# Kernel tuning notes

Measured on AMD Instinct MI355X. Metric: run time of the kernel, lower is better.

The kernel has to match this reference:

```python
import jax, jax.numpy as jnp
import numpy as np

N_EMBD = 1024
HEAD_SIZE = 64


def setup_inputs() -> dict:
    key = jax.random.key(0)
    kx, kq, kk, kv = jax.random.split(key, 4)
    B, T = 8, 2048
    x = jax.random.normal(kx, (B, T, N_EMBD), dtype=jnp.float32)
    s = 1.0 / np.sqrt(N_EMBD)
    Wq = jax.random.normal(kq, (N_EMBD, HEAD_SIZE), dtype=jnp.float32) * s
    Wk = jax.random.normal(kk, (N_EMBD, HEAD_SIZE), dtype=jnp.float32) * s
    Wv = jax.random.normal(kv, (N_EMBD, HEAD_SIZE), dtype=jnp.float32) * s
    return {"x": x, "Wq": Wq, "Wk": Wk, "Wv": Wv}


def reference(x, Wq, Wk, Wv):
    # x: [B, T, C]; W*: [C, H]
    q = jnp.einsum('btc,ch->bth', x, Wq)
    k = jnp.einsum('btc,ch->bth', x, Wk)
    v = jnp.einsum('btc,ch->bth', x, Wv)
    H = q.shape[-1]
    score = jnp.einsum('bth,bsh->bts', q, k) / jnp.sqrt(jnp.asarray(H, q.dtype))
    T = score.shape[-1]
    causal = jnp.tril(jnp.ones((T, T), dtype=bool))  # [T, T]
    score = jnp.where(causal, score, -jnp.inf)
    attn = jax.nn.softmax(score, axis=-1)
    return jnp.einsum('bts,bsh->bth', attn, v)
```

## Files before the change

kernel.cpp:

```cpp
#include <hip/hip_runtime.h>

typedef __bf16 bf16;
typedef __attribute__((ext_vector_type(8))) __bf16 bf16x8;
typedef __attribute__((ext_vector_type(4))) __bf16 bf16x4;
typedef __attribute__((ext_vector_type(4))) float floatx4;

#define MFMA16(a, b, c) __builtin_amdgcn_mfma_f32_16x16x32_bf16((a), (b), (c), 0, 0, 0)

__global__ void prep_w(const float* __restrict__ Wq, const float* __restrict__ Wk,
                       const float* __restrict__ Wv, bf16* __restrict__ wTf) {
    int tid = blockIdx.x * 256 + threadIdx.x;
    int j = tid & 7;
    int l = (tid >> 3) & 15;
    int q = (tid >> 7) & 3;
    int kc = (tid >> 9) & 31;
    int mt = tid >> 14;
    int mat = mt >> 2;
    int h = ((mt & 3) << 4) + l;
    int c = kc * 32 + q * 8 + j;
    const float* W = (mat == 0) ? Wq : (mat == 1) ? Wk : Wv;
    wTf[tid] = (bf16)W[c * 64 + h];
}

#define XSTR 1032

__global__ __launch_bounds__(256, 4) void proj_qkv(const float* __restrict__ x,
                                                   const bf16* __restrict__ wTf,
                                                   bf16* __restrict__ q,
                                                   bf16* __restrict__ k,
                                                   bf16* __restrict__ vT) {
    __shared__ bf16 xs[16 * XSTR];

    const int tid = threadIdx.x;
    const int lane = tid & 63;
    const int w = tid >> 6;
    const int l15 = lane & 15;
    const int quad = lane >> 4;
    const int T0 = blockIdx.x * 16;

    {
        const int r = tid >> 4;
        const int cm = tid & 15;
        const float* g = x + (size_t)(T0 + r) * 1024 + cm * 8;
        floatx4 f[16];
        #pragma unroll
        for (int c = 0; c < 8; c++) {
            f[2 * c]     = *(const floatx4*)(g + c * 128);
            f[2 * c + 1] = *(const floatx4*)(g + c * 128 + 4);
        }
        bf16* ld = xs + r * XSTR + cm * 8;
        #pragma unroll
        for (int c = 0; c < 8; c++) {
            bf16x8 pk;
            pk[0] = (bf16)f[2*c][0]; pk[1] = (bf16)f[2*c][1];
            pk[2] = (bf16)f[2*c][2]; pk[3] = (bf16)f[2*c][3];
            pk[4] = (bf16)f[2*c+1][0]; pk[5] = (bf16)f[2*c+1][1];
            pk[6] = (bf16)f[2*c+1][2]; pk[7] = (bf16)f[2*c+1][3];
            *(bf16x8*)(ld + c * 128) = pk;
        }
    }
    __syncthreads();

    floatx4 acc[3] = {};
    const bf16* aw0 = wTf + (size_t)(w * 3 + 0) * 16384 + lane * 8;
    const bf16* aw1 = wTf + (size_t)(w * 3 + 1) * 16384 + lane * 8;
    const bf16* aw2 = wTf + (size_t)(w * 3 + 2) * 16384 + lane * 8;
    const bf16* xr = xs + l15 * XSTR + quad * 8;

    bf16x8 a0c = *(const bf16x8*)(aw0);
    bf16x8 a1c = *(const bf16x8*)(aw1);
    bf16x8 a2c = *(const bf16x8*)(aw2);
    bf16x8 a0n = *(const bf16x8*)(aw0 + 512);
    bf16x8 a1n = *(const bf16x8*)(aw1 + 512);
    bf16x8 a2n = *(const bf16x8*)(aw2 + 512);

    #pragma unroll 4
    for (int kc = 0; kc < 32; kc++) {
        bf16x8 p0 = *(const bf16x8*)(aw0 + (kc + 2) * 512);
        bf16x8 p1 = *(const bf16x8*)(aw1 + (kc + 2) * 512);
        bf16x8 p2 = *(const bf16x8*)(aw2 + (kc + 2) * 512);
        bf16x8 bb = *(const bf16x8*)(xr + kc * 32);
        acc[0] = MFMA16(a0c, bb, acc[0]);
        acc[1] = MFMA16(a1c, bb, acc[1]);
        acc[2] = MFMA16(a2c, bb, acc[2]);
        a0c = a0n; a1c = a1n; a2c = a2n;
        a0n = p0;  a1n = p1;  a2n = p2;
    }

    const int t = T0 + l15;
    #pragma unroll
    for (int i = 0; i < 3; i++) {
        int mtile = w * 3 + i;
        int mat = mtile >> 2;
        int hbase = ((mtile & 3) << 4) + (quad << 2);
        float sc = (mat == 0) ? 0.125f : 1.0f;
        bf16x4 pk;
        pk[0] = (bf16)(acc[i][0] * sc);
        pk[1] = (bf16)(acc[i][1] * sc);
        pk[2] = (bf16)(acc[i][2] * sc);
        pk[3] = (bf16)(acc[i][3] * sc);
        if (mat == 0) {
            *(bf16x4*)(q + (size_t)t * 64 + hbase) = pk;
        } else if (mat == 1) {
            *(bf16x4*)(k + (size_t)t * 64 + hbase) = pk;
        } else {
            int b = t >> 11, tt = t & 2047;
            #pragma unroll
            for (int r = 0; r < 4; r++)
                vT[(size_t)(b * 64 + hbase + r) * 2048 + tt] = pk[r];
        }
    }
}

#define KP2 72
#define OH 68

__global__ __launch_bounds__(512, 4) void flash(const bf16* __restrict__ q,
                                                const bf16* __restrict__ k,
                                                const bf16* __restrict__ vT,
                                                float* __restrict__ out) {
    __shared__ char smem[8 * 16 * OH * 4];
    __shared__ float Ms[8][16], Ls[8][16];
    bf16* psall = (bf16*)smem;
    float* Os = (float*)smem;

    const int b = blockIdx.x & 7;
    const int p = blockIdx.x >> 3;
    const int t0A = p * 16;
    const int t0B = (127 - p) * 16;
    const int nttA = (p >> 2) + 1;
    const int nttB = ((127 - p) >> 2) + 1;
    const int L = nttA + nttB;

    const int tid = threadIdx.x;
    const int w = tid >> 6;
    const int lane = tid & 63;
    const int l15 = lane & 15;
    const int quad = lane >> 4;

    const int s0 = (L * w) >> 3;
    const int s1 = (L * (w + 1)) >> 3;

    const bf16* kbase = k + (size_t)(b * 2048 + l15) * 64 + quad * 8;
    const bf16* vbase = vT + (size_t)(b * 64 + l15) * 2048 + quad * 8;
    bf16* psw = psall + w * 16 * KP2;

    const bf16* qpA = q + (size_t)(b * 2048 + t0A + l15) * 64 + quad * 8;
    const bf16* qpB = q + (size_t)(b * 2048 + t0B + l15) * 64 + quad * 8;

    floatx4 oA[4] = {}, oB[4] = {};
    float miA = -1e30f, liA = 0.f, miB = -1e30f, liB = 0.f;

#define KV_STEP(jtv, isdiag, t0v, qf0v, qf1v, mi_, li_, o_)                          \
    {                                                                                 \
        const bf16* kp = kbase + (size_t)(jtv) * 4096;                                \
        floatx4 stt[4];                                                               \
        _Pragma("unroll") for (int mt = 0; mt < 4; mt++) {                            \
            floatx4 z = {};                                                           \
            bf16x8 ka0 = *(const bf16x8*)(kp + mt * 1024);                            \
            bf16x8 ka1 = *(const bf16x8*)(kp + mt * 1024 + 32);                       \
            z = MFMA16(ka0, qf0v, z);                                                 \
            z = MFMA16(ka1, qf1v, z);                                                 \
            stt[mt] = z;                                                              \
        }                                                                             \
        if (isdiag) {                                                                 \
            _Pragma("unroll") for (int mt = 0; mt < 4; mt++)                          \
                _Pragma("unroll") for (int r = 0; r < 4; r++) {                       \
                    int kv = (jtv) * 64 + mt * 16 + quad * 4 + r;                     \
                    if (kv > (t0v) + l15) stt[mt][r] = -1e30f;                        \
                }                                                                     \
        }                                                                             \
        float mx = fmaxf(fmaxf(fmaxf(stt[0][0], stt[0][1]), fmaxf(stt[0][2], stt[0][3])),  \
                         fmaxf(fmaxf(stt[1][0], stt[1][1]), fmaxf(stt[1][2], stt[1][3]))); \
        mx = fmaxf(mx, fmaxf(fmaxf(fmaxf(stt[2][0], stt[2][1]), fmaxf(stt[2][2], stt[2][3])),  \
                             fmaxf(fmaxf(stt[3][0], stt[3][1]), fmaxf(stt[3][2], stt[3][3])))); \
        mx = fmaxf(mx, __shfl_xor(mx, 16, 64));                                       \
        mx = fmaxf(mx, __shfl_xor(mx, 32, 64));                                       \
        float mnew = fmaxf(mi_, mx);                                                  \
        float aa = __expf(mi_ - mnew);                                                \
        mi_ = mnew;                                                                   \
        float rs = 0.f;                                                               \
        _Pragma("unroll") for (int mt = 0; mt < 4; mt++)                              \
            _Pragma("unroll") for (int r = 0; r < 4; r++) {                           \
                float pv = __expf(stt[mt][r] - mnew);                                 \
                stt[mt][r] = pv;                                                      \
                rs += pv;                                                             \
            }                                                                         \
        rs += __shfl_xor(rs, 16, 64);                                                 \
        rs += __shfl_xor(rs, 32, 64);                                                 \
        li_ = li_ * aa + rs;                                                          \
        _Pragma("unroll") for (int mt = 0; mt < 4; mt++)                              \
            _Pragma("unroll") for (int r = 0; r < 4; r++) o_[mt][r] *= aa;            \
        _Pragma("unroll") for (int mt = 0; mt < 4; mt++) {                            \
            bf16x4 pk;                                                                \
            pk[0] = (bf16)stt[mt][0]; pk[1] = (bf16)stt[mt][1];                       \
            pk[2] = (bf16)stt[mt][2]; pk[3] = (bf16)stt[mt][3];                       \
            *(bf16x4*)(psw + l15 * KP2 + mt * 16 + quad * 4) = pk;                    \
        }                                                                             \
        const bf16* vp = vbase + (jtv) * 64;                                          \
        _Pragma("unroll") for (int kc = 0; kc < 2; kc++) {                            \
            bf16x8 pb = *(const bf16x8*)(psw + l15 * KP2 + kc * 32 + quad * 8);       \
            _Pragma("unroll") for (int mt = 0; mt < 4; mt++) {                        \
                bf16x8 va = *(const bf16x8*)(vp + mt * 32768 + kc * 32);              \
                o_[mt] = MFMA16(va, pb, o_[mt]);                                      \
            }                                                                         \
        }                                                                             \
    }

    {
        const int eA = (s1 < nttA) ? s1 : nttA;
        if (s0 < eA) {
            bf16x8 qf0 = *(const bf16x8*)qpA;
            bf16x8 qf1 = *(const bf16x8*)(qpA + 32);
            for (int s = s0; s < eA; s++) {
                KV_STEP(s, (s == nttA - 1), t0A, qf0, qf1, miA, liA, oA);
            }
        }
    }
    {
        const int sB = (s0 > nttA) ? s0 : nttA;
        if (sB < s1) {
            bf16x8 qf0 = *(const bf16x8*)qpB;
            bf16x8 qf1 = *(const bf16x8*)(qpB + 32);
            for (int s = sB; s < s1; s++) {
                KV_STEP(s - nttA, (s == L - 1), t0B, qf0, qf1, miB, liB, oB);
            }
        }
    }

    #pragma unroll
    for (int tile = 0; tile < 2; tile++) {
        __syncthreads();
        float mi = tile ? miB : miA;
        float li = tile ? liB : liA;
        if (lane < 16) { Ms[w][lane] = mi; Ls[w][lane] = li; }
        #pragma unroll
        for (int mt = 0; mt < 4; mt++) {
            floatx4 ov = tile ? oB[mt] : oA[mt];
            *(floatx4*)(Os + (w * 16 + l15) * OH + mt * 16 + quad * 4) = ov;
        }
        __syncthreads();
        {
            int qq = tid >> 5;
            int h2 = (tid & 31) * 2;
            float Mg = -1e30f;
            #pragma unroll
            for (int u = 0; u < 8; u++) Mg = fmaxf(Mg, Ms[u][qq]);
            float Lg = 0.f, v0 = 0.f, v1 = 0.f;
            #pragma unroll
            for (int u = 0; u < 8; u++) {
                float sw = __expf(Ms[u][qq] - Mg);
                Lg += sw * Ls[u][qq];
                const float* Or = Os + (u * 16 + qq) * OH + h2;
                v0 += sw * Or[0];
                v1 += sw * Or[1];
            }
            float inv = 1.0f / Lg;
            int t0v = tile ? t0B : t0A;
            float* op = out + (size_t)(b * 2048 + t0v + qq) * 64 + h2;
            op[0] = v0 * inv;
            op[1] = v1 * inv;
        }
    }
#undef KV_STEP
}

extern "C" void kernel_launch(void* const* d_in, const int* in_sizes, int n_in,
                              void* d_out, int out_size, void* d_ws, size_t ws_size,
                              hipStream_t stream) {
    const float* x  = (const float*)d_in[0];
    const float* Wq = (const float*)d_in[1];
    const float* Wk = (const float*)d_in[2];
    const float* Wv = (const float*)d_in[3];
    float* out = (float*)d_out;

    char* ws = (char*)d_ws;
    bf16* wTf = (bf16*)ws;
    bf16* q   = (bf16*)(ws + 397312);
    bf16* k   = (bf16*)(ws + 397312 + 2097152);
    bf16* vT  = (bf16*)(ws + 397312 + 2 * 2097152);

    hipLaunchKernelGGL(prep_w,   dim3(768),  dim3(256), 0, stream, Wq, Wk, Wv, wTf);
    hipLaunchKernelGGL(proj_qkv, dim3(1024), dim3(256), 0, stream, x, wTf, q, k, vT);
    hipLaunchKernelGGL(flash,    dim3(512),  dim3(512), 0, stream, q, k, vT, out);
}
```

Baseline: 144.2 us.

## Software-pipeline K tile loads and merge two-tile attention loops into one

The two per-tile KV loops become a single loop over both query tiles. The K fragments for the next step are prefetched into registers while the current step's softmax and PV MFMAs run. Q fragments for both tiles are loaded up front. Nontemporal hints are added to the x loads in the projection and to the final output stores. Selecting tile state at runtime (oA/oB through a pointer, mi/li via ternaries) may force the accumulators into scratch memory or add extra register pressure.

```diff
diff --git a/kernel.cpp b/kernel.cpp
--- a/kernel.cpp
+++ b/kernel.cpp
@@ -45,8 +45,8 @@
         floatx4 f[16];
         #pragma unroll
         for (int c = 0; c < 8; c++) {
-            f[2 * c]     = *(const floatx4*)(g + c * 128);
-            f[2 * c + 1] = *(const floatx4*)(g + c * 128 + 4);
+            f[2 * c]     = __builtin_nontemporal_load((const floatx4*)(g + c * 128));
+            f[2 * c + 1] = __builtin_nontemporal_load((const floatx4*)(g + c * 128 + 4));
         }
         bf16* ld = xs + r * XSTR + cm * 8;
         #pragma unroll
@@ -147,83 +147,109 @@
 
     const bf16* qpA = q + (size_t)(b * 2048 + t0A + l15) * 64 + quad * 8;
     const bf16* qpB = q + (size_t)(b * 2048 + t0B + l15) * 64 + quad * 8;
+    bf16x8 qfA0 = *(const bf16x8*)qpA;
+    bf16x8 qfA1 = *(const bf16x8*)(qpA + 32);
+    bf16x8 qfB0 = *(const bf16x8*)qpB;
+    bf16x8 qfB1 = *(const bf16x8*)(qpB + 32);
 
     floatx4 oA[4] = {}, oB[4] = {};
     float miA = -1e30f, liA = 0.f, miB = -1e30f, liB = 0.f;
 
-#define KV_STEP(jtv, isdiag, t0v, qf0v, qf1v, mi_, li_, o_)                          \
-    {                                                                                 \
-        const bf16* kp = kbase + (size_t)(jtv) * 4096;                                \
-        floatx4 stt[4];                                                               \
-        _Pragma("unroll") for (int mt = 0; mt < 4; mt++) {                            \
-            floatx4 z = {};                                                           \
-            bf16x8 ka0 = *(const bf16x8*)(kp + mt * 1024);                            \
-            bf16x8 ka1 = *(const bf16x8*)(kp + mt * 1024 + 32);                       \
-            z = MFMA16(ka0, qf0v, z);                                                 \
-            z = MFMA16(ka1, qf1v, z);                                                 \
-            stt[mt] = z;                                                              \
-        }                                                                             \
-        if (isdiag) {                                                                 \
-            _Pragma("unroll") for (int mt = 0; mt < 4; mt++)                          \
-                _Pragma("unroll") for (int r = 0; r < 4; r++) {                       \
-                    int kv = (jtv) * 64 + mt * 16 + quad * 4 + r;                     \
-                    if (kv > (t0v) + l15) stt[mt][r] = -1e30f;                        \
-                }                                                                     \
-        }                                                                             \
-        float mx = fmaxf(fmaxf(fmaxf(stt[0][0], stt[0][1]), fmaxf(stt[0][2], stt[0][3])),  \
-                         fmaxf(fmaxf(stt[1][0], stt[1][1]), fmaxf(stt[1][2], stt[1][3]))); \
-        mx = fmaxf(mx, fmaxf(fmaxf(fmaxf(stt[2][0], stt[2][1]), fmaxf(stt[2][2], stt[2][3])),  \
-                             fmaxf(fmaxf(stt[3][0], stt[3][1]), fmaxf(stt[3][2], stt[3][3])))); \
-        mx = fmaxf(mx, __shfl_xor(mx, 16, 64));                                       \
-        mx = fmaxf(mx, __shfl_xor(mx, 32, 64));                                       \
-        float mnew = fmaxf(mi_, mx);                                                  \
-        float aa = __expf(mi_ - mnew);                                                \
-        mi_ = mnew;                                                                   \
-        float rs = 0.f;                                                               \
-        _Pragma("unroll") for (int mt = 0; mt < 4; mt++)                              \
-            _Pragma("unroll") for (int r = 0; r < 4; r++) {                           \
-                float pv = __expf(stt[mt][r] - mnew);                                 \
-                stt[mt][r] = pv;                                                      \
-                rs += pv;                                                             \
-            }                                                                         \
-        rs += __shfl_xor(rs, 16, 64);                                                 \
-        rs += __shfl_xor(rs, 32, 64);                                                 \
-        li_ = li_ * aa + rs;                                                          \
-        _Pragma("unroll") for (int mt = 0; mt < 4; mt++)                              \
-            _Pragma("unroll") for (int r = 0; r < 4; r++) o_[mt][r] *= aa;            \
-        _Pragma("unroll") for (int mt = 0; mt < 4; mt++) {                            \
-            bf16x4 pk;                                                                \
-            pk[0] = (bf16)stt[mt][0]; pk[1] = (bf16)stt[mt][1];                       \
-            pk[2] = (bf16)stt[mt][2]; pk[3] = (bf16)stt[mt][3];                       \
-            *(bf16x4*)(psw + l15 * KP2 + mt * 16 + quad * 4) = pk;                    \
-        }                                                                             \
-        const bf16* vp = vbase + (jtv) * 64;                                          \
-        _Pragma("unroll") for (int kc = 0; kc < 2; kc++) {                            \
-            bf16x8 pb = *(const bf16x8*)(psw + l15 * KP2 + kc * 32 + quad * 8);       \
-            _Pragma("unroll") for (int mt = 0; mt < 4; mt++) {                        \
-                bf16x8 va = *(const bf16x8*)(vp + mt * 32768 + kc * 32);              \
-                o_[mt] = MFMA16(va, pb, o_[mt]);                                      \
-            }                                                                         \
-        }                                                                             \
-    }
-
+    auto jt_of = [&](int s) { return (s < nttA) ? s : (s - nttA); };
+
+    bf16x8 kf[8];
     {
-        const int eA = (s1 < nttA) ? s1 : nttA;
-        if (s0 < eA) {
-            bf16x8 qf0 = *(const bf16x8*)qpA;
-            bf16x8 qf1 = *(const bf16x8*)(qpA + 32);
-            for (int s = s0; s < eA; s++) {
-                KV_STEP(s, (s == nttA - 1), t0A, qf0, qf1, miA, liA, oA);
+        const bf16* kp = kbase + (size_t)jt_of(s0) * 4096;
+        #pragma unroll
+        for (int mt = 0; mt < 4; mt++) {
+            kf[2 * mt]     = *(const bf16x8*)(kp + mt * 1024);
+            kf[2 * mt + 1] = *(const bf16x8*)(kp + mt * 1024 + 32);
+        }
+    }
+
+    for (int s = s0; s < s1; s++) {
+        const bool tileA = (s < nttA);
+        const int jt = tileA ? s : (s - nttA);
+        const int t0v = tileA ? t0A : t0B;
+        const bool isdiag = tileA ? (s == nttA - 1) : (s == L - 1);
+        bf16x8 qf0 = tileA ? qfA0 : qfB0;
+        bf16x8 qf1 = tileA ? qfA1 : qfB1;
+
+        floatx4 stt[4];
+        #pragma unroll
+        for (int mt = 0; mt < 4; mt++) {
+            floatx4 z = {};
+            z = MFMA16(kf[2 * mt], qf0, z);
+            z = MFMA16(kf[2 * mt + 1], qf1, z);
+            stt[mt] = z;
+        }
+
+        if (s + 1 < s1) {
+            const bf16* kp = kbase + (size_t)jt_of(s + 1) * 4096;
+            #pragma unroll
+            for (int mt = 0; mt < 4; mt++) {
+                kf[2 * mt]     = *(const bf16x8*)(kp + mt * 1024);
+                kf[2 * mt + 1] = *(const bf16x8*)(kp + mt * 1024 + 32);
             }
         }
-    }
-    {
-        const int sB = (s0 > nttA) ? s0 : nttA;
-        if (sB < s1) {
-            bf16x8 qf0 = *(const bf16x8*)qpB;
-            bf16x8 qf1 = *(const bf16x8*)(qpB + 32);
-            for (int s = sB; s < s1; s++) {
-                KV_STEP(s - nttA, (s == L - 1), t0B, qf0, qf1, miB, liB, oB);
+
+        if (isdiag) {
+            #pragma unroll
+            for (int mt = 0; mt < 4; mt++)
+                #pragma unroll
+                for (int r = 0; r < 4; r++) {
+                    int kv = jt * 64 + mt * 16 + quad * 4 + r;
+                    if (kv > t0v + l15) stt[mt][r] = -1e30f;
+                }
+        }
+
+        float mx = fmaxf(fmaxf(fmaxf(stt[0][0], stt[0][1]), fmaxf(stt[0][2], stt[0][3])),
+                         fmaxf(fmaxf(stt[1][0], stt[1][1]), fmaxf(stt[1][2], stt[1][3])));
+        mx = fmaxf(mx, fmaxf(fmaxf(fmaxf(stt[2][0], stt[2][1]), fmaxf(stt[2][2], stt[2][3])),
+                             fmaxf(fmaxf(stt[3][0], stt[3][1]), fmaxf(stt[3][2], stt[3][3]))));
+        mx = fmaxf(mx, __shfl_xor(mx, 16, 64));
+        mx = fmaxf(mx, __shfl_xor(mx, 32, 64));
+
+        float mi = tileA ? miA : miB;
+        float li = tileA ? liA : liB;
+        float mnew = fmaxf(mi, mx);
+        float aa = __expf(mi - mnew);
+        float rs = 0.f;
+        #pragma unroll
+        for (int mt = 0; mt < 4; mt++)
+            #pragma unroll
+            for (int r = 0; r < 4; r++) {
+                float pv = __expf(stt[mt][r] - mnew);
+                stt[mt][r] = pv;
+                rs += pv;
+            }
+        rs += __shfl_xor(rs, 16, 64);
+        rs += __shfl_xor(rs, 32, 64);
+        if (tileA) { miA = mnew; liA = liA * aa + rs; }
+        else       { miB = mnew; liB = liB * aa + rs; }
+
+        floatx4* o = tileA ? oA : oB;
+        #pragma unroll
+        for (int mt = 0; mt < 4; mt++)
+            #pragma unroll
+            for (int r = 0; r < 4; r++) o[mt][r] *= aa;
+
+        #pragma unroll
+        for (int mt = 0; mt < 4; mt++) {
+            bf16x4 pk;
+            pk[0] = (bf16)stt[mt][0]; pk[1] = (bf16)stt[mt][1];
+            pk[2] = (bf16)stt[mt][2]; pk[3] = (bf16)stt[mt][3];
+            *(bf16x4*)(psw + l15 * KP2 + mt * 16 + quad * 4) = pk;
+        }
+
+        const bf16* vp = vbase + jt * 64;
+        #pragma unroll
+        for (int kc = 0; kc < 2; kc++) {
+            bf16x8 pb = *(const bf16x8*)(psw + l15 * KP2 + kc * 32 + quad * 8);
+            #pragma unroll
+            for (int mt = 0; mt < 4; mt++) {
+                bf16x8 va = *(const bf16x8*)(vp + mt * 32768 + kc * 32);
+                o[mt] = MFMA16(va, pb, o[mt]);
             }
         }
     }
@@ -258,11 +284,10 @@
             float inv = 1.0f / Lg;
             int t0v = tile ? t0B : t0A;
             float* op = out + (size_t)(b * 2048 + t0v + qq) * 64 + h2;
-            op[0] = v0 * inv;
-            op[1] = v1 * inv;
-        }
-    }
-#undef KV_STEP
+            __builtin_nontemporal_store(v0 * inv, op);
+            __builtin_nontemporal_store(v1 * inv, op + 1);
+        }
+    }
 }
 
 extern "C" void kernel_launch(void* const* d_in, const int* in_sizes, int n_in,
```

Measured after the change: 177.2 us. 1.23x slower.
